# Performance work log

Measured on AMD Instinct MI355X. Metric: run time of the kernel, lower is better.

The kernel has to match this reference:

```python
import jax, jax.numpy as jnp
import numpy as np

EPS_RMS = 1e-6
EPS_SCALE = 1e-5


def setup_inputs() -> dict:
    key = jax.random.key(0)
    k1, k2 = jax.random.split(key)
    B, S, D_IN, D_OUT = 4, 2048, 2048, 8192
    x = jax.random.normal(k1, (B, S, D_IN), dtype=jnp.float32)
    # kaiming_uniform-ish init bound
    bound = 1.0 / np.sqrt(D_IN)
    weight = jax.random.uniform(k2, (D_OUT, D_IN), dtype=jnp.float32, minval=-bound, maxval=bound)
    gamma = jnp.ones((D_IN,), dtype=jnp.float32)
    return {"x": x, "weight": weight, "gamma": gamma}


def rmsnorm(x, gamma):
    xf = x.astype(jnp.float32)
    inv = jax.lax.rsqrt(jnp.mean(xf * xf, axis=-1, keepdims=True) + EPS_RMS)
    return (xf * inv).astype(x.dtype) * gamma


def quantize_weights_ternary(weight):
    scale = jnp.maximum(jnp.mean(jnp.abs(weight)), EPS_SCALE)
    wn = weight / scale
    wq = jax.lax.stop_gradient(jnp.round(jnp.clip(wn, -1.0, 1.0)) - wn) + wn  # STE
    return wq, scale


def reference(x, weight, gamma):
    x_norm = rmsnorm(x, gamma)                      # [B, S, D_in]
    wq, scale = quantize_weights_ternary(weight)    # [D_out, D_in], scalar
    out = jnp.einsum('bsd,od->bso', x_norm, wq)     # [B, S, D_out]
    return out * scale
```

## Files before the change

### kernel.cpp

```cpp
#include <hip/hip_runtime.h>
#include <hip/hip_bf16.h>
#include <stdint.h>

#define M_ROWS 8192
#define K_DIM  2048
#define N_DIM  8192
#define W_ELEMS (N_DIM * K_DIM)
#define X_ELEMS (M_ROWS * K_DIM)
#define NT 32
#define ABSUM_BLOCKS 256

typedef __bf16 v8bf __attribute__((ext_vector_type(8)));
typedef float  v4f  __attribute__((ext_vector_type(4)));

__device__ inline unsigned short f2bf(float f) {
  uint32_t u = __builtin_bit_cast(uint32_t, f);
  uint32_t r = (u + 0x7fffu + ((u >> 16) & 1u)) >> 16;
  return (unsigned short)r;
}

__device__ inline void async_copy16(const void* g, void* l) {
  __builtin_amdgcn_global_load_lds(
      (const __attribute__((address_space(1))) void*)g,
      (__attribute__((address_space(3))) void*)l, 16, 0, 0);
}

__device__ inline float scale_from_partials(const double* __restrict__ partials) {
  const int lane = threadIdx.x & 63;
  double d = partials[lane] + partials[lane + 64] +
             partials[lane + 128] + partials[lane + 192];
  for (int off = 32; off > 0; off >>= 1) d += __shfl_down(d, off);
  d = __shfl(d, 0);
  return (float)fmax(d * (1.0 / (double)W_ELEMS), 1e-5);
}

__global__ __launch_bounds__(256) void prep_kernel(const float* __restrict__ X,
                                                   const float* __restrict__ gamma,
                                                   const float* __restrict__ W,
                                                   unsigned short* __restrict__ Xn,
                                                   double* __restrict__ partials) {
  __shared__ double wsumd[4];
  __shared__ float wsumf[4];
  const int t = threadIdx.x;
  const int lane = t & 63, wid = t >> 6;

  if (blockIdx.x < ABSUM_BLOCKS) {
    const int pb = blockIdx.x;
    int tid = pb * 256 + t;
    const float4* W4 = (const float4*)W;
    const int n4 = W_ELEMS / 4;
    double acc = 0.0;
    for (int i = tid; i < n4; i += ABSUM_BLOCKS * 256) {
      float4 v = W4[i];
      acc += (double)fabsf(v.x) + (double)fabsf(v.y) +
             (double)fabsf(v.z) + (double)fabsf(v.w);
    }
    for (int off = 32; off > 0; off >>= 1) acc += __shfl_down(acc, off);
    if (lane == 0) wsumd[wid] = acc;
    __syncthreads();
    if (t == 0) partials[pb] = wsumd[0] + wsumd[1] + wsumd[2] + wsumd[3];
    return;
  }

  const int row = blockIdx.x - ABSUM_BLOCKS;
  const float4* xr = (const float4*)(X + (size_t)row * K_DIM);
  float4 a = xr[t];
  float4 b = xr[t + 256];
  float ss = a.x * a.x + a.y * a.y + a.z * a.z + a.w * a.w +
             b.x * b.x + b.y * b.y + b.z * b.z + b.w * b.w;
  for (int off = 32; off > 0; off >>= 1) ss += __shfl_down(ss, off);
  if (lane == 0) wsumf[wid] = ss;
  __syncthreads();
  float total = wsumf[0] + wsumf[1] + wsumf[2] + wsumf[3];
  float inv = 1.0f / sqrtf(total * (1.0f / (float)K_DIM) + 1e-6f);
  const float4* gr = (const float4*)gamma;
  float4 g0 = gr[t];
  float4 g1 = gr[t + 256];
  union { unsigned short h[4]; uint2 u; } pa, pb;
  pa.h[0] = f2bf((a.x * inv) * g0.x);
  pa.h[1] = f2bf((a.y * inv) * g0.y);
  pa.h[2] = f2bf((a.z * inv) * g0.z);
  pa.h[3] = f2bf((a.w * inv) * g0.w);
  pb.h[0] = f2bf((b.x * inv) * g1.x);
  pb.h[1] = f2bf((b.y * inv) * g1.y);
  pb.h[2] = f2bf((b.z * inv) * g1.z);
  pb.h[3] = f2bf((b.w * inv) * g1.w);
  uint2* orow = (uint2*)(Xn + (size_t)row * K_DIM);
  orow[t] = pa.u;
  orow[t + 256] = pb.u;
}

__global__ __launch_bounds__(256) void quant_kernel(const float* __restrict__ W,
                                                    const double* __restrict__ partials,
                                                    float* __restrict__ scale_out,
                                                    unsigned short* __restrict__ Wq) {
  const float s = scale_from_partials(partials);
  const int t = threadIdx.x;
  if (blockIdx.x == 0 && t == 0) scale_out[0] = s;
  const float4* W4 = (const float4*)W + (size_t)blockIdx.x * 512;
  float4 a = W4[t];
  float4 b = W4[t + 256];
  union { unsigned short h[4]; uint2 u; } pa, pb;
  pa.h[0] = f2bf(rintf(fminf(1.f, fmaxf(-1.f, a.x / s))));
  pa.h[1] = f2bf(rintf(fminf(1.f, fmaxf(-1.f, a.y / s))));
  pa.h[2] = f2bf(rintf(fminf(1.f, fmaxf(-1.f, a.z / s))));
  pa.h[3] = f2bf(rintf(fminf(1.f, fmaxf(-1.f, a.w / s))));
  pb.h[0] = f2bf(rintf(fminf(1.f, fmaxf(-1.f, b.x / s))));
  pb.h[1] = f2bf(rintf(fminf(1.f, fmaxf(-1.f, b.y / s))));
  pb.h[2] = f2bf(rintf(fminf(1.f, fmaxf(-1.f, b.z / s))));
  pb.h[3] = f2bf(rintf(fminf(1.f, fmaxf(-1.f, b.w / s))));
  uint2* o = (uint2*)(Wq + (size_t)blockIdx.x * 2048);
  o[t] = pa.u;
  o[t + 256] = pb.u;
}

__global__ __launch_bounds__(512, 2) void gemm_kernel(
    const unsigned short* __restrict__ A,
    const unsigned short* __restrict__ B,
    const float* __restrict__ scale,
    float* __restrict__ C) {
  __shared__ __align__(16) char lds[131072];

  const int tid = threadIdx.x;
  const int lane = tid & 63;
  const int wave = tid >> 6;
  const int wm = wave & 1;
  const int wn = wave >> 1;

  const int bid = blockIdx.x;
  const int swz = (bid & 7) * 128 + (bid >> 3);
  const int st = swz >> 4, wi = swz & 15;
  const int mb = (st >> 3) * 4 + (wi >> 2);
  const int nb = (st & 7) * 4 + (wi & 3);
  const int m0 = mb * 256;
  const int n0 = nb * 256;

  const int srow3 = lane >> 3;
  const int scg = (lane & 7) ^ srow3;

  const int aoff_a = wm * 8192 + (lane & 15) * 128;
  const int boff_b = wn * 4096 + (lane & 15) * 128;
  const int swzk0 = ((lane >> 4) ^ (lane & 7)) << 4;
  const int swzk1 = ((4 + (lane >> 4)) ^ (lane & 7)) << 4;

  v4f acc[8][4] = {};
  v8bf af[4][2];
  v8bf b0f[2][2];
  v8bf b1f[2][2];

#define STAGE_A(B_, H_, KT_) do {                                              \
    _Pragma("unroll")                                                          \
    for (int j = 0; j < 2; ++j) {                                              \
      const int chunk_ = wave * 2 + j;                                         \
      const int slot_ = chunk_ * 8 + srow3;                                    \
      const int row_ = ((slot_ >> 6) << 7) + ((H_) << 6) + (slot_ & 63);       \
      async_copy16(A + (size_t)(m0 + row_) * K_DIM + ((KT_) << 6) + (scg << 3),\
                   lds + (B_) * 32768 + (H_) * 16384 + chunk_ * 1024);         \
    } } while (0)

#define STAGE_B(B_, H_, KT_) do {                                              \
    _Pragma("unroll")                                                          \
    for (int j = 0; j < 2; ++j) {                                              \
      const int chunk_ = wave * 2 + j;                                         \
      const int slot_ = chunk_ * 8 + srow3;                                    \
      const int row_ = ((slot_ >> 5) << 6) + ((H_) << 5) + (slot_ & 31);       \
      async_copy16(B + (size_t)(n0 + row_) * K_DIM + ((KT_) << 6) + (scg << 3),\
                   lds + 65536 + (B_) * 32768 + (H_) * 16384 + chunk_ * 1024); \
    } } while (0)

#define LOADA(B_, QM_) do {                                                    \
    _Pragma("unroll")                                                          \
    for (int tm = 0; tm < 4; ++tm) {                                           \
      af[tm][0] = *(const v8bf*)(lds + (B_) * 32768 + (QM_) * 16384 +          \
                                 aoff_a + tm * 2048 + swzk0);                  \
      af[tm][1] = *(const v8bf*)(lds + (B_) * 32768 + (QM_) * 16384 +          \
                                 aoff_a + tm * 2048 + swzk1);                  \
    } } while (0)

#define LOADB(B_, QN_, DST) do {                                               \
    _Pragma("unroll")                                                          \
    for (int tn = 0; tn < 2; ++tn) {                                           \
      DST[tn][0] = *(const v8bf*)(lds + 65536 + (B_) * 32768 + (QN_) * 16384 + \
                                  boff_b + tn * 2048 + swzk0);                 \
      DST[tn][1] = *(const v8bf*)(lds + 65536 + (B_) * 32768 + (QN_) * 16384 + \
                                  boff_b + tn * 2048 + swzk1);                 \
    } } while (0)

#define MMAC(BF, QM_, QN_) do {                                                \
    _Pragma("unroll")                                                          \
    for (int ks = 0; ks < 2; ++ks)                                             \
    _Pragma("unroll")                                                          \
    for (int tm = 0; tm < 4; ++tm)                                             \
    _Pragma("unroll")                                                          \
    for (int tn = 0; tn < 2; ++tn)                                             \
      acc[(QM_) * 4 + tm][(QN_) * 2 + tn] =                                    \
          __builtin_amdgcn_mfma_f32_16x16x32_bf16(                             \
              BF[tn][ks], af[tm][ks],                                          \
              acc[(QM_) * 4 + tm][(QN_) * 2 + tn], 0, 0, 0);                   \
  } while (0)

#define BAR()    __builtin_amdgcn_s_barrier()
#define SCHED0() __builtin_amdgcn_sched_barrier(0)
#define VMG6()   asm volatile("s_waitcnt vmcnt(6)" ::: "memory")

#define PHASE(READS_, STAGE_, MM_) do {                                        \
    READS_;                                                                    \
    STAGE_;                                                                    \
    BAR();                                                                     \
    __builtin_amdgcn_s_setprio(1); MM_;                                        \
    __builtin_amdgcn_s_setprio(0);                                             \
    VMG6(); BAR(); SCHED0();                                                   \
  } while (0)

#define TILE(T_, B_) do {                                                      \
    const int t1_ = ((T_) + 1 < NT) ? (T_) + 1 : NT - 1;                       \
    const int t2_ = ((T_) + 2 < NT) ? (T_) + 2 : NT - 1;                       \
    PHASE(LOADA(B_, 0),            STAGE_A(1 - (B_), 0, t1_), MMAC(b0f, 0, 0));\
    PHASE(LOADB(B_, 1, b1f),       STAGE_B(1 - (B_), 1, t1_), MMAC(b1f, 0, 1));\
    PHASE(LOADA(B_, 1),            STAGE_A(1 - (B_), 1, t1_), MMAC(b0f, 1, 0));\
    PHASE(LOADB(1 - (B_), 0, b0f), STAGE_B(B_, 0, t2_),       MMAC(b1f, 1, 1));\
  } while (0)

  STAGE_B(0, 0, 0);
  STAGE_A(0, 0, 0);
  STAGE_B(0, 1, 0);
  STAGE_A(0, 1, 0);
  STAGE_B(1, 0, 1);
  VMG6();
  BAR(); SCHED0();
  LOADB(0, 0, b0f);

  for (int t = 0; t < NT; t += 2) {
    TILE(t, 0);
    TILE(t + 1, 1);
  }

  const float s = scale[0];
  const int mBase = m0 + wm * 128 + (lane & 15);
  const int nBase = n0 + wn * 64 + ((lane >> 4) << 2);
#pragma unroll
  for (int tm = 0; tm < 8; ++tm) {
#pragma unroll
    for (int tn = 0; tn < 4; ++tn) {
      float4 v;
      v.x = acc[tm][tn][0] * s;
      v.y = acc[tm][tn][1] * s;
      v.z = acc[tm][tn][2] * s;
      v.w = acc[tm][tn][3] * s;
      *(float4*)&C[(size_t)(mBase + tm * 16) * N_DIM + (nBase + tn * 16)] = v;
    }
  }

#undef STAGE_A
#undef STAGE_B
#undef LOADA
#undef LOADB
#undef MMAC
#undef BAR
#undef SCHED0
#undef VMG6
#undef PHASE
#undef TILE
}

extern "C" void kernel_launch(void* const* d_in, const int* in_sizes, int n_in,
                              void* d_out, int out_size, void* d_ws, size_t ws_size,
                              hipStream_t stream) {
  const float* x = (const float*)d_in[0];
  const float* w = (const float*)d_in[1];
  const float* gamma = (const float*)d_in[2];
  float* out = (float*)d_out;

  float* scale_f = (float*)d_ws;
  unsigned short* xn = (unsigned short*)((char*)d_ws + 16);
  unsigned short* wq = (unsigned short*)((char*)d_ws + 16 + (size_t)X_ELEMS * 2);
  double* partials = (double*)out;

  prep_kernel<<<ABSUM_BLOCKS + M_ROWS, 256, 0, stream>>>(x, gamma, w, xn, partials);
  quant_kernel<<<W_ELEMS / 2048, 256, 0, stream>>>(w, partials, scale_f, wq);
  gemm_kernel<<<(M_ROWS / 256) * (N_DIM / 256), 512, 0, stream>>>(xn, wq, scale_f, out);
}
```

Before: 598.9 us.

## Double-buffer A/B register fragments so LDS reads prefetch one phase ahead

Restructures the per-tile phase schedule so that each phase's LDS fragment reads feed the next phase's MFMAs. It adds a second A fragment buffer and ping-pong B0 buffers, and stages the first A half of the next tile early. The aim is to hide LDS read latency behind MFMA work instead of loading and consuming fragments in the same phase. It costs extra VGPRs (more fragment registers), which could lower occupancy or cause spills, and it changes the vmcnt wait pattern, with a final vmcnt(0) added.

```diff
diff --git a/kernel.cpp b/kernel.cpp
--- a/kernel.cpp
+++ b/kernel.cpp
@@ -145,7 +145,9 @@
 
   v4f acc[8][4] = {};
   v8bf af[4][2];
-  v8bf b0f[2][2];
+  v8bf af2[4][2];
+  v8bf b0fA[2][2];
+  v8bf b0fB[2][2];
   v8bf b1f[2][2];
 
 #define STAGE_A(B_, H_, KT_) do {                                              \
@@ -168,13 +170,13 @@
                    lds + 65536 + (B_) * 32768 + (H_) * 16384 + chunk_ * 1024); \
     } } while (0)
 
-#define LOADA(B_, QM_) do {                                                    \
+#define LOADA(B_, QM_, DST) do {                                               \
     _Pragma("unroll")                                                          \
     for (int tm = 0; tm < 4; ++tm) {                                           \
-      af[tm][0] = *(const v8bf*)(lds + (B_) * 32768 + (QM_) * 16384 +          \
-                                 aoff_a + tm * 2048 + swzk0);                  \
-      af[tm][1] = *(const v8bf*)(lds + (B_) * 32768 + (QM_) * 16384 +          \
-                                 aoff_a + tm * 2048 + swzk1);                  \
+      DST[tm][0] = *(const v8bf*)(lds + (B_) * 32768 + (QM_) * 16384 +         \
+                                  aoff_a + tm * 2048 + swzk0);                 \
+      DST[tm][1] = *(const v8bf*)(lds + (B_) * 32768 + (QM_) * 16384 +         \
+                                  aoff_a + tm * 2048 + swzk1);                 \
     } } while (0)
 
 #define LOADB(B_, QN_, DST) do {                                               \
@@ -186,7 +188,7 @@
                                   boff_b + tn * 2048 + swzk1);                 \
     } } while (0)
 
-#define MMAC(BF, QM_, QN_) do {                                                \
+#define MMAC(BF, AF, QM_, QN_) do {                                            \
     _Pragma("unroll")                                                          \
     for (int ks = 0; ks < 2; ++ks)                                             \
     _Pragma("unroll")                                                          \
@@ -195,30 +197,35 @@
     for (int tn = 0; tn < 2; ++tn)                                             \
       acc[(QM_) * 4 + tm][(QN_) * 2 + tn] =                                    \
           __builtin_amdgcn_mfma_f32_16x16x32_bf16(                             \
-              BF[tn][ks], af[tm][ks],                                          \
+              BF[tn][ks], AF[tm][ks],                                          \
               acc[(QM_) * 4 + tm][(QN_) * 2 + tn], 0, 0, 0);                   \
   } while (0)
 
 #define BAR()    __builtin_amdgcn_s_barrier()
 #define SCHED0() __builtin_amdgcn_sched_barrier(0)
 #define VMG6()   asm volatile("s_waitcnt vmcnt(6)" ::: "memory")
+#define PRIO1()  __builtin_amdgcn_s_setprio(1)
+#define PRIO0()  __builtin_amdgcn_s_setprio(0)
 
 #define PHASE(READS_, STAGE_, MM_) do {                                        \
     READS_;                                                                    \
     STAGE_;                                                                    \
     BAR();                                                                     \
-    __builtin_amdgcn_s_setprio(1); MM_;                                        \
-    __builtin_amdgcn_s_setprio(0);                                             \
+    PRIO1(); MM_; PRIO0();                                                     \
     VMG6(); BAR(); SCHED0();                                                   \
   } while (0)
 
-#define TILE(T_, B_) do {                                                      \
+#define TILE(T_, B_, BCUR, BNXT) do {                                          \
     const int t1_ = ((T_) + 1 < NT) ? (T_) + 1 : NT - 1;                       \
     const int t2_ = ((T_) + 2 < NT) ? (T_) + 2 : NT - 1;                       \
-    PHASE(LOADA(B_, 0),            STAGE_A(1 - (B_), 0, t1_), MMAC(b0f, 0, 0));\
-    PHASE(LOADB(B_, 1, b1f),       STAGE_B(1 - (B_), 1, t1_), MMAC(b1f, 0, 1));\
-    PHASE(LOADA(B_, 1),            STAGE_A(1 - (B_), 1, t1_), MMAC(b0f, 1, 0));\
-    PHASE(LOADB(1 - (B_), 0, b0f), STAGE_B(B_, 0, t2_),       MMAC(b1f, 1, 1));\
+    PHASE(LOADB(B_, 1, b1f),        STAGE_B(1 - (B_), 1, t1_),                 \
+          MMAC(BCUR, af, 0, 0));                                               \
+    PHASE(LOADA(B_, 1, af2),        STAGE_A(1 - (B_), 1, t1_),                 \
+          MMAC(b1f, af, 0, 1));                                                \
+    PHASE(LOADB(1 - (B_), 0, BNXT), STAGE_B(B_, 0, t2_),                       \
+          MMAC(BCUR, af2, 1, 0));                                              \
+    PHASE(LOADA(1 - (B_), 0, af),   STAGE_A(B_, 0, t2_),                       \
+          MMAC(b1f, af2, 1, 1));                                               \
   } while (0)
 
   STAGE_B(0, 0, 0);
@@ -226,14 +233,18 @@
   STAGE_B(0, 1, 0);
   STAGE_A(0, 1, 0);
   STAGE_B(1, 0, 1);
+  STAGE_A(1, 0, 1);
   VMG6();
   BAR(); SCHED0();
-  LOADB(0, 0, b0f);
+  LOADB(0, 0, b0fA);
+  LOADA(0, 0, af);
 
   for (int t = 0; t < NT; t += 2) {
-    TILE(t, 0);
-    TILE(t + 1, 1);
+    TILE(t, 0, b0fA, b0fB);
+    TILE(t + 1, 1, b0fB, b0fA);
   }
+
+  asm volatile("s_waitcnt vmcnt(0)" ::: "memory");
 
   const float s = scale[0];
   const int mBase = m0 + wm * 128 + (lane & 15);
@@ -259,6 +270,8 @@
 #undef BAR
 #undef SCHED0
 #undef VMG6
+#undef PRIO1
+#undef PRIO0
 #undef PHASE
 #undef TILE
 }
```

Measured after the change: 853.4 us. 1.42x slower.
